# Kernel tuning notes

Measured on AMD Instinct MI355X. Metric: run time of the kernel, lower is better.

The kernel has to match this reference:

```python
import jax, jax.numpy as jnp
import numpy as np

# RoIAlign 2D config (matches init_kwargs)
OUT_H, OUT_W = 7, 7
SPATIAL_SCALE = 0.25
S = 2  # sampling_ratio: S x S sample points per output bin
N, C, H, W = 4, 256, 200, 200
R = 512


def setup_inputs() -> dict:
    key = jax.random.key(0)
    k1, k2, k3, k4, k5 = jax.random.split(key, 5)
    features = jax.random.normal(k1, (N, C, H, W), dtype=jnp.float32)
    # rois in image coordinates (image is H/scale = 800 px): (batch_idx, x1, y1, x2, y2)
    img = H / SPATIAL_SCALE
    b = jax.random.randint(k2, (R,), 0, N).astype(jnp.float32)
    xy1 = jax.random.uniform(k3, (R, 2), dtype=jnp.float32, maxval=img - 96.0)
    wh = jax.random.uniform(k4, (R, 2), dtype=jnp.float32, minval=16.0, maxval=96.0)
    rois = jnp.concatenate([b[:, None], xy1, xy1 + wh], axis=1)  # [R,5]
    return {"features": features, "rois": rois}


def _axis_weights(start, bin_size, out_size, limit):
    """Per-axis sample coords -> (low/high indices [R,out*S,2], lerp weights [R,out*S,2]).
    Matches mmdet/torchvision RoIAlign CUDA kernel semantics."""
    # sample coordinate: start + (i + 0.5) * bin / S  ==  start + ph*bin + (iy+0.5)*bin/S
    i = (jnp.arange(out_size * S, dtype=jnp.float32) + 0.5) / S
    y = start[:, None] + i[None, :] * bin_size[:, None]          # [R, out*S]
    valid = (y >= -1.0) & (y <= limit)                            # kernel: skip if y<-1 or y>H
    yc = jnp.clip(y, 0.0, limit - 1.0)
    yl = jnp.floor(yc).astype(jnp.int32)                          # in [0, H-1]
    yh = jnp.minimum(yl + 1, limit - 1)
    l = yc - yl.astype(jnp.float32)                               # 0 at the top edge, as in kernel
    w = jnp.stack([1.0 - l, l], axis=-1) * valid[..., None].astype(jnp.float32)  # [R,out*S,2]
    idx = jnp.stack([yl, yh], axis=-1)                            # [R,out*S,2]
    return idx, w


def reference(features, rois):
    # order=1 (bilinear) path of RoIAlign2DFunction
    b = rois[:, 0].astype(jnp.int32)                              # [R]
    x1, y1, x2, y2 = (rois[:, k] * SPATIAL_SCALE for k in (1, 2, 3, 4))
    roi_w = jnp.maximum(x2 - x1, 1.0)
    roi_h = jnp.maximum(y2 - y1, 1.0)
    bin_w = roi_w / OUT_W
    bin_h = roi_h / OUT_H

    yidx, wy = _axis_weights(y1, bin_h, OUT_H, H)                 # [R,Hs,2]
    xidx, wx = _axis_weights(x1, bin_w, OUT_W, W)                 # [R,Ws,2]

    nhwc = jnp.transpose(features, (0, 2, 3, 1))                  # [N,H,W,C]
    # gather 2x2 bilinear neighbors for every sample point: [R,Hs,Ws,2,2,C]
    vals = nhwc[b[:, None, None, None, None],
                yidx[:, :, None, :, None],
                xidx[:, None, :, None, :]]
    samples = jnp.einsum('rhwabc,rha,rwb->rhwc', vals, wy, wx)    # [R,Hs,Ws,C]
    Hs, Ws = OUT_H * S, OUT_W * S
    pooled = samples.reshape(R, OUT_H, S, OUT_W, S, C).mean(axis=(2, 4))  # avg over S*S points
    return jnp.transpose(pooled, (0, 3, 1, 2))                    # [R,C,out_h,out_w]
```

## Files before the change

kernel.cpp:

```cpp
#include <hip/hip_runtime.h>


typedef float f4 __attribute__((ext_vector_type(4)));

#define OH 7
#define OW 7
#define NSAMP 14
#define CH 256
#define FH 200
#define FW 200
#define NR 512
#define CCH 16
#define NCHUNK (CH / CCH)
#define MAXFY 25
#define MAXFX 28
#define BLK 256

__global__ __launch_bounds__(BLK) void roialign_fwd(
    const float* __restrict__ feat,
    const float* __restrict__ rois,
    float* __restrict__ out)
{
    __shared__ __align__(16) float tile[MAXFY * MAXFX * CCH];
    __shared__ int   s_il[2][NSAMP];
    __shared__ int   s_ih[2][NSAMP];
    __shared__ float s_w0[2][NSAMP];
    __shared__ float s_w1[2][NSAMP];

    const int block = blockIdx.x;
    const int r     = block >> 4;
    const int c0    = (block & (NCHUNK - 1)) * CCH;
    const int tid   = threadIdx.x;

    const int   b  = (int)rois[r * 5 + 0];
    const float x1 = rois[r * 5 + 1] * 0.25f;
    const float y1 = rois[r * 5 + 2] * 0.25f;
    const float x2 = rois[r * 5 + 3] * 0.25f;
    const float y2 = rois[r * 5 + 4] * 0.25f;
    const float bw = fmaxf(x2 - x1, 1.0f) * (1.0f / OW);
    const float bh = fmaxf(y2 - y1, 1.0f) * (1.0f / OH);

    if (tid < 2 * NSAMP) {
        const int axis = tid >= NSAMP;
        const int i    = tid - axis * NSAMP;
        const float start = axis ? x1 : y1;
        const float bsz   = axis ? bw : bh;
        const float pos   = start + (i + 0.5f) * 0.5f * bsz;
        const float valid = (pos >= -1.0f && pos <= 200.0f) ? 1.0f : 0.0f;
        const float pc    = fminf(fmaxf(pos, 0.0f), 199.0f);
        const int   il    = (int)floorf(pc);
        const int   ih    = min(il + 1, 199);
        const float l     = pc - (float)il;
        s_il[axis][i] = il;
        s_ih[axis][i] = ih;
        s_w0[axis][i] = (1.0f - l) * valid;
        s_w1[axis][i] = l * valid;
    }
    __syncthreads();

    const int ylo = s_il[0][0];
    const int xlo = s_il[1][0] & ~3;
    const int fh  = min(s_ih[0][NSAMP - 1] - ylo + 1, MAXFY);
    const int fwa = min(s_ih[1][NSAMP - 1] - xlo + 1, MAXFX);

    {
        const int fwv = (fwa + 3) >> 2;
        const int mgk = (1048576 + fwv - 1) / fwv;
        const int total = fh * CCH * fwv;
        const float* fb = feat + ((size_t)(b * CH + c0) * FH + ylo) * FW + xlo;
        for (int w = tid; w < total; w += BLK) {
            const int row = (int)(((unsigned)(w * mgk)) >> 20);
            const int xv  = w - row * fwv;
            const int cc  = row & 15;
            const int y   = row >> 4;
            const int xs  = min(4 * xv, fwa - 4);
            const f4 v = *(const f4*)(fb + ((size_t)cc * FH + y) * FW + xs);
            const int p0 = y * fwa + xs;
            #pragma unroll
            for (int j = 0; j < 4; j++) {
                const int p  = p0 + j;
                const int cs = (cc + 4 * ((p >> 2) & 3)) & 15;
                tile[p * CCH + cs] = v[j];
            }
        }
    }
    __syncthreads();

    if (tid < 4 * OH * OW) {
        const int q   = tid & 3;
        const int bin = tid >> 2;
        const int ph  = bin / OW;
        const int pw  = bin - ph * OW;
        f4 acc = {0.0f, 0.0f, 0.0f, 0.0f};
        #pragma unroll
        for (int sy = 0; sy < 2; sy++) {
            const int gy = ph * 2 + sy;
            const int rl = (s_il[0][gy] - ylo) * fwa;
            const int rh = (s_ih[0][gy] - ylo) * fwa;
            const float wy0 = s_w0[0][gy];
            const float wy1 = s_w1[0][gy];
            #pragma unroll
            for (int sx = 0; sx < 2; sx++) {
                const int gx = pw * 2 + sx;
                const int il = s_il[1][gx] - xlo;
                const int ih = s_ih[1][gx] - xlo;
                const float wx0 = s_w0[1][gx];
                const float wx1 = s_w1[1][gx];
                const float w00 = wy0 * wx0, w01 = wy0 * wx1;
                const float w10 = wy1 * wx0, w11 = wy1 * wx1;
                const int p00 = rl + il, p01 = rl + ih;
                const int p10 = rh + il, p11 = rh + ih;
                const f4 v00 = *(const f4*)(tile + p00 * CCH + 4 * ((q + (p00 >> 2)) & 3));
                const f4 v01 = *(const f4*)(tile + p01 * CCH + 4 * ((q + (p01 >> 2)) & 3));
                const f4 v10 = *(const f4*)(tile + p10 * CCH + 4 * ((q + (p10 >> 2)) & 3));
                const f4 v11 = *(const f4*)(tile + p11 * CCH + 4 * ((q + (p11 >> 2)) & 3));
                acc += w00 * v00 + w01 * v01 + w10 * v10 + w11 * v11;
            }
        }
        acc *= 0.25f;
        float* o = out + ((size_t)r * CH + c0 + 4 * q) * (OH * OW) + bin;
        o[0 * OH * OW] = acc.x;
        o[1 * OH * OW] = acc.y;
        o[2 * OH * OW] = acc.z;
        o[3 * OH * OW] = acc.w;
    }
}

extern "C" void kernel_launch(void* const* d_in, const int* in_sizes, int n_in,
                              void* d_out, int out_size, void* d_ws, size_t ws_size,
                              hipStream_t stream) {
    const float* feat = (const float*)d_in[0];
    const float* rois = (const float*)d_in[1];
    float* out = (float*)d_out;
    roialign_fwd<<<NR * NCHUNK, BLK, 0, stream>>>(feat, rois, out);
}
```

Baseline: 252.5 us.

## Sort RoIs spatially and map channel chunks to XCDs for cache locality

Adds a single-block bitonic sort kernel that orders RoIs by batch and a serpentine spatial cell key. The main kernel remaps block indices so each XCD (blockIdx & 7) handles two fixed channel chunks and walks RoIs in sorted order. The aim is for overlapping RoIs touching the same feature slice to run close together on the same XCD, so feature tiles hit in L2 instead of being fetched again from HBM. The cost is an extra serialized kernel launch plus an indirection load, and the mapping assumes 8 XCDs with round-robin block dispatch.

New measurement: 259.3 us. +2.7%, slower.

```diff
diff --git a/kernel.cpp b/kernel.cpp
--- a/kernel.cpp
+++ b/kernel.cpp
@@ -16,9 +16,43 @@
 #define MAXFX 28
 #define BLK 256
 
+__global__ __launch_bounds__(256) void roi_sort(
+    const float* __restrict__ rois, int* __restrict__ perm)
+{
+    __shared__ unsigned skey[NR];
+    const int t = threadIdx.x;
+    for (int i = t; i < NR; i += 256) {
+        const int   b  = (int)rois[i * 5 + 0];
+        const float cx = (rois[i * 5 + 1] + rois[i * 5 + 3]) * 0.125f;
+        const float cy = (rois[i * 5 + 2] + rois[i * 5 + 4]) * 0.125f;
+        int xc = (int)(cx * (1.0f / 14.0f));
+        int yc = (int)(cy * (1.0f / 14.0f));
+        xc = min(15, max(0, xc));
+        yc = min(15, max(0, yc));
+        const int xs = (yc & 1) ? (15 - xc) : xc;
+        skey[i] = ((((unsigned)b * 16u + yc) * 16u + xs) << 10) | (unsigned)i;
+    }
+    __syncthreads();
+    for (int k = 2; k <= NR; k <<= 1) {
+        for (int j = k >> 1; j > 0; j >>= 1) {
+            for (int i = t; i < NR; i += 256) {
+                const int ixj = i ^ j;
+                if (ixj > i) {
+                    const bool up = ((i & k) == 0);
+                    const unsigned a = skey[i], c = skey[ixj];
+                    if ((a > c) == up) { skey[i] = c; skey[ixj] = a; }
+                }
+            }
+            __syncthreads();
+        }
+    }
+    for (int i = t; i < NR; i += 256) perm[i] = (int)(skey[i] & 1023u);
+}
+
 __global__ __launch_bounds__(BLK) void roialign_fwd(
     const float* __restrict__ feat,
     const float* __restrict__ rois,
+    const int* __restrict__ perm,
     float* __restrict__ out)
 {
     __shared__ __align__(16) float tile[MAXFY * MAXFX * CCH];
@@ -27,9 +61,12 @@
     __shared__ float s_w0[2][NSAMP];
     __shared__ float s_w1[2][NSAMP];
 
-    const int block = blockIdx.x;
-    const int r     = block >> 4;
-    const int c0    = (block & (NCHUNK - 1)) * CCH;
+    const int xcd   = blockIdx.x & 7;
+    const int seq   = blockIdx.x >> 3;
+    const int chunk = xcd * 2 + (seq >> 9);
+    const int spos  = seq & (NR - 1);
+    const int r     = perm[spos];
+    const int c0    = chunk * CCH;
     const int tid   = threadIdx.x;
 
     const int   b  = (int)rois[r * 5 + 0];
@@ -132,5 +169,7 @@
     const float* feat = (const float*)d_in[0];
     const float* rois = (const float*)d_in[1];
     float* out = (float*)d_out;
-    roialign_fwd<<<NR * NCHUNK, BLK, 0, stream>>>(feat, rois, out);
+    int* perm = (int*)d_ws;
+    roi_sort<<<1, 256, 0, stream>>>(rois, perm);
+    roialign_fwd<<<NR * NCHUNK, BLK, 0, stream>>>(feat, rois, perm, out);
 }
```
